# Performance work log

Measured on AMD Instinct MI355X. Metric: run time of the kernel, lower is better.

## Reference

```python
import jax, jax.numpy as jnp
import numpy as np

N = 100000      # nodes
E = 1600000     # directed edges (before self loops)
IN_DIM = 5
HID = 64
NEG_SLOPE = 0.2  # PyG GATConv default LeakyReLU slope


def setup_inputs() -> dict:
    key = jax.random.key(0)
    ks = jax.random.split(key, 12)
    x = jax.random.normal(ks[0], (N, IN_DIM), dtype=jnp.float32)
    edge_index = jax.random.randint(ks[1], (2, E), 0, N, dtype=jnp.int64)
    # layer 1 params (GATConv(5, HID), heads=1)
    W1 = jax.random.normal(ks[2], (IN_DIM, HID), dtype=jnp.float32) * (1.0 / np.sqrt(IN_DIM))
    a_src1 = jax.random.normal(ks[3], (HID,), dtype=jnp.float32) * 0.1
    a_dst1 = jax.random.normal(ks[4], (HID,), dtype=jnp.float32) * 0.1
    b1 = jnp.zeros((HID,), dtype=jnp.float32)
    # layer 2 params (GATConv(HID, 1))
    W2 = jax.random.normal(ks[5], (HID, 1), dtype=jnp.float32) * (1.0 / np.sqrt(HID))
    a_src2 = jax.random.normal(ks[6], (1,), dtype=jnp.float32) * 0.1
    a_dst2 = jax.random.normal(ks[7], (1,), dtype=jnp.float32) * 0.1
    b2 = jnp.zeros((1,), dtype=jnp.float32)
    return {"x": x, "edge_index": edge_index,
            "W1": W1, "a_src1": a_src1, "a_dst1": a_dst1, "b1": b1,
            "W2": W2, "a_src2": a_src2, "a_dst2": a_dst2, "b2": b2}


def _gat_layer(x, W, a_src, a_dst, b, src, dst):
    h = x @ W                                   # [N, F]
    s_src = h @ a_src                           # [N] per-node src score
    s_dst = h @ a_dst                           # [N] per-node dst score
    e = s_src[src] + s_dst[dst]                 # [E'] edge logits
    e = jnp.where(e > 0, e, NEG_SLOPE * e)      # LeakyReLU(0.2)
    # segment softmax over incoming edges of each dst node
    m = jax.ops.segment_max(e, dst, num_segments=N)
    ex = jnp.exp(e - m[dst])
    denom = jax.ops.segment_sum(ex, dst, num_segments=N)
    coef = ex / denom[dst]                      # [E'] attention coefficients
    out = jax.ops.segment_sum(coef[:, None] * h[src], dst, num_segments=N)
    return out + b


def reference(x, edge_index, W1, a_src1, a_dst1, b1, W2, a_src2, a_dst2, b2):
    si = jnp.arange(N, dtype=edge_index.dtype)  # add self loops (PyG default)
    src = jnp.concatenate([edge_index[0], si])
    dst = jnp.concatenate([edge_index[1], si])
    h = _gat_layer(x, W1, a_src1, a_dst1, b1, src, dst)
    h = jax.nn.relu(h)
    return _gat_layer(h, W2, a_src2, a_dst2, b2, src, dst)  # [N, 1]
```

## Files before the change

kernel.cpp:

```cpp
#include <hip/hip_runtime.h>
#include <hip/hip_bf16.h>
#include <hip/hip_fp16.h>

#define NN 100000
#define EE 1600000
#define ET (EE + NN)
#define HID 64
#define NEG 0.2f
#define NBUK 391
#define SCT_TILE 8192
#define BUKCAP 8192

__device__ __forceinline__ float uh(unsigned u) {
    __half_raw r; r.x = (unsigned short)(u & 0xFFFF);
    return __half2float(__half(r));
}
__device__ __forceinline__ unsigned f2h(float f) {
    __half h = __float2half_rn(f);
    __half_raw r = *reinterpret_cast<__half_raw*>(&h);
    return (unsigned)r.x;
}

__global__ __launch_bounds__(256) void k_proj(const float* __restrict__ x,
                                              const float* __restrict__ W1,
                                              const float* __restrict__ a_src1,
                                              const float* __restrict__ a_dst1,
                                              unsigned* __restrict__ rec,
                                              float* __restrict__ sd1,
                                              int* __restrict__ bcur) {
    if (blockIdx.x == 0) {
        for (int i = threadIdx.x; i < 1024; i += 256) bcur[i] = 0;
    }
    int wid  = threadIdx.x >> 6;
    int lane = threadIdx.x & 63;
    int half = lane >> 5, li = lane & 31;
    int n = (blockIdx.x * 4 + wid) * 2 + half;
    if (n >= NN) return;
    float xv[5];
    float h0 = 0.f, h1 = 0.f;
#pragma unroll
    for (int k = 0; k < 5; ++k) {
        xv[k] = x[n * 5 + k];
        h0 += xv[k] * W1[k * HID + li];
        h1 += xv[k] * W1[k * HID + li + 32];
    }
    float a = h0 * a_src1[li] + h1 * a_src1[li + 32];
    float b = h0 * a_dst1[li] + h1 * a_dst1[li + 32];
#pragma unroll
    for (int o = 1; o <= 16; o <<= 1) { a += __shfl_xor(a, o); b += __shfl_xor(b, o); }
    if (li == 0) {
        sd1[n] = b;
        uint4 rv;
        rv.x = __float_as_uint(a);
        rv.y = f2h(xv[0]) | (f2h(xv[1]) << 16);
        rv.z = f2h(xv[2]) | (f2h(xv[3]) << 16);
        rv.w = f2h(xv[4]);
        *(uint4*)(rec + (size_t)n * 4) = rv;
    }
}

__global__ __launch_bounds__(512) void k_bscatter(const int* __restrict__ ei,
                                                  int* __restrict__ bcur,
                                                  unsigned* __restrict__ pairs) {
    __shared__ unsigned sp[SCT_TILE];
    __shared__ unsigned short bid[SCT_TILE];
    __shared__ int cnt_[NBUK], loc[NBUK], cur[NBUK];
    __shared__ int wsum[8];
    int tid = threadIdx.x;
    int wid = tid >> 6, lane = tid & 63;
    int base = blockIdx.x * SCT_TILE;
    int tilecnt = ET - base; if (tilecnt > SCT_TILE) tilecnt = SCT_TILE;

    for (int i = tid; i < NBUK; i += 512) cnt_[i] = 0;
    __syncthreads();
    int sreg[16], dreg[16], rreg[16];
#pragma unroll
    for (int it = 0; it < 4; ++it) {
        int i = base + (it * 512 + tid) * 4;
        if (i + 3 < EE) {
            const int4 sv = *(const int4*)(ei + i);
            const int4 dv = *(const int4*)(ei + EE + i);
            sreg[it*4+0] = sv.x; sreg[it*4+1] = sv.y; sreg[it*4+2] = sv.z; sreg[it*4+3] = sv.w;
            dreg[it*4+0] = dv.x; dreg[it*4+1] = dv.y; dreg[it*4+2] = dv.z; dreg[it*4+3] = dv.w;
        } else {
#pragma unroll
            for (int k = 0; k < 4; ++k) {
                int idx = i + k;
                if (idx < EE)      { sreg[it*4+k] = ei[idx];  dreg[it*4+k] = ei[EE + idx]; }
                else if (idx < ET) { sreg[it*4+k] = idx - EE; dreg[it*4+k] = idx - EE; }
                else               { dreg[it*4+k] = -1; }
            }
        }
#pragma unroll
        for (int k = 0; k < 4; ++k)
            if (dreg[it*4+k] >= 0) rreg[it*4+k] = atomicAdd(&cnt_[dreg[it*4+k] >> 8], 1);
    }
    __syncthreads();
    int b0 = tid * 4;
    int s0 = 0;
    if (b0 < NBUK)
        for (int k = 0; k < 4 && b0 + k < NBUK; ++k) s0 += cnt_[b0 + k];
    int incl = s0;
#pragma unroll
    for (int o = 1; o < 64; o <<= 1) {
        int t = __shfl(incl, (lane - o) & 63);
        if (lane >= o) incl += t;
    }
    if (lane == 63) wsum[wid] = incl;
    __syncthreads();
    int wpref = 0;
    for (int w = 0; w < wid; ++w) wpref += wsum[w];
    if (b0 < NBUK) {
        int run = wpref + incl - s0;
        for (int k = 0; k < 4 && b0 + k < NBUK; ++k) {
            loc[b0 + k] = run;
            run += cnt_[b0 + k];
        }
    }
    __syncthreads();
    for (int i = tid; i < NBUK; i += 512) {
        int c = cnt_[i];
        cur[i] = c ? (atomicAdd(&bcur[i], c) + i * BUKCAP - loc[i]) : 0;
    }
    __syncthreads();
#pragma unroll
    for (int q = 0; q < 16; ++q) {
        if (dreg[q] >= 0) {
            int s = sreg[q], d = dreg[q];
            int b = d >> 8;
            int slot = loc[b] + rreg[q];
            sp[slot]  = ((unsigned)(d & 255) << 17) | (unsigned)s;
            bid[slot] = (unsigned short)b;
        }
    }
    __syncthreads();
    for (int i = tid; i < tilecnt; i += 512)
        pairs[cur[bid[i]] + i] = sp[i];
}

__global__ __launch_bounds__(1024) void k_bsort(const int* __restrict__ bcur,
                                                unsigned* __restrict__ pairs,
                                                int* __restrict__ rowptr,
                                                int* __restrict__ cntd) {
    __shared__ int hist[256], sc[256];
    int b = blockIdx.x;
    int cnt = bcur[b];
    if (cnt > BUKCAP) cnt = BUKCAP;
    int base = b * BUKCAP;
    int tid = threadIdx.x;
    if (tid < 256) hist[tid] = 0;
    __syncthreads();
    unsigned preg[8];
    int rreg[8];
    int i0 = tid * 8;
    if (i0 + 8 <= cnt) {
        const uint4 v0 = *(const uint4*)(pairs + base + i0);
        const uint4 v1 = *(const uint4*)(pairs + base + i0 + 4);
        preg[0] = v0.x; preg[1] = v0.y; preg[2] = v0.z; preg[3] = v0.w;
        preg[4] = v1.x; preg[5] = v1.y; preg[6] = v1.z; preg[7] = v1.w;
    } else {
#pragma unroll
        for (int j = 0; j < 8; ++j)
            preg[j] = (i0 + j < cnt) ? pairs[base + i0 + j] : 0xFFFFFFFFu;
    }
#pragma unroll
    for (int j = 0; j < 8; ++j)
        if (preg[j] != 0xFFFFFFFFu) rreg[j] = atomicAdd(&hist[preg[j] >> 17], 1);
    __syncthreads();
    if (tid < 64) {
        int v0 = hist[4 * tid], v1 = hist[4 * tid + 1];
        int v2 = hist[4 * tid + 2], v3 = hist[4 * tid + 3];
        int s = v0 + v1 + v2 + v3;
#pragma unroll
        for (int o = 1; o < 64; o <<= 1) {
            int t = __shfl(s, (tid - o) & 63);
            if (tid >= o) s += t;
        }
        int excl = s - v0 - v1 - v2 - v3;
        sc[4 * tid]     = excl;
        sc[4 * tid + 1] = excl + v0;
        sc[4 * tid + 2] = excl + v0 + v1;
        sc[4 * tid + 3] = excl + v0 + v1 + v2;
    }
    __syncthreads();
    int nbase = b << 8;
    if (tid < 256 && nbase + tid < NN) {
        rowptr[nbase + tid] = base + sc[tid];
        cntd[nbase + tid]   = hist[tid];
    }
    int* adj = (int*)pairs;
#pragma unroll
    for (int j = 0; j < 8; ++j) {
        if (preg[j] != 0xFFFFFFFFu) {
            int ld = (int)(preg[j] >> 17);
            adj[base + sc[ld] + rreg[j]] = (int)(preg[j] & 0x1FFFF);
        }
    }
}

__device__ __forceinline__ void agg1_node_gen(int n, int lane,
                                              const int* __restrict__ rowptr,
                                              const int* __restrict__ cntd,
                                              const int* __restrict__ adj,
                                              const unsigned* __restrict__ rec,
                                              const float* __restrict__ sd1,
                                              const float* __restrict__ W1,
                                              const float* __restrict__ b1,
                                              const float* __restrict__ W2,
                                              float* __restrict__ h2) {
    int off = rowptr[n], deg = cntd[n];
    float sdn = sd1[n];
    float dsum = 0.f, a0 = 0.f, a1 = 0.f, a2 = 0.f, a3 = 0.f, a4 = 0.f;
    for (int j0 = 0; j0 < deg; j0 += 64) {
        int j = j0 + lane;
        if (j < deg) {
            int s = adj[off + j];
            const uint4 v = *(const uint4*)(rec + (size_t)s * 4);
            float t = __uint_as_float(v.x) + sdn;
            float e = t > 0.f ? t : NEG * t;
            float w = __expf(e);
            dsum += w;
            a0 += w * uh(v.y); a1 += w * uh(v.y >> 16);
            a2 += w * uh(v.z); a3 += w * uh(v.z >> 16);
            a4 += w * uh(v.w);
        }
    }
#pragma unroll
    for (int o = 32; o; o >>= 1) {
        dsum += __shfl_xor(dsum, o);
        a0 += __shfl_xor(a0, o); a1 += __shfl_xor(a1, o); a2 += __shfl_xor(a2, o);
        a3 += __shfl_xor(a3, o); a4 += __shfl_xor(a4, o);
    }
    float inv = 1.0f / dsum;
    a0 *= inv; a1 *= inv; a2 *= inv; a3 *= inv; a4 *= inv;
    float of = b1[lane] + a0 * W1[lane] + a1 * W1[64 + lane] + a2 * W1[128 + lane]
             + a3 * W1[192 + lane] + a4 * W1[256 + lane];
    of = fmaxf(of, 0.f);
    float p2 = of * W2[lane];
#pragma unroll
    for (int o = 32; o; o >>= 1) p2 += __shfl_xor(p2, o);
    if (lane == 0) h2[n] = p2;
}

__global__ __launch_bounds__(256) void k_agg1(const int* __restrict__ rowptr,
                                              const int* __restrict__ cntd,
                                              const int* __restrict__ adj,
                                              const unsigned* __restrict__ rec,
                                              const float* __restrict__ sd1,
                                              const float* __restrict__ W1,
                                              const float* __restrict__ b1,
                                              const float* __restrict__ W2,
                                              float* __restrict__ h2) {
    int wid  = threadIdx.x >> 6;
    int lane = threadIdx.x & 63;
    int n0 = (blockIdx.x * 4 + wid) * 2;
    if (n0 >= NN) return;
    int d0 = cntd[n0], d1 = cntd[n0 + 1];

    if (d0 <= 32 && d1 <= 32) {
        int half = lane >> 5, li = lane & 31;
        int n = n0 + half;
        int off = rowptr[n];
        int deg = half ? d1 : d0;
        float sdn = sd1[n];
        int s = adj[off + (li < deg ? li : 0)];
        const uint4 v = *(const uint4*)(rec + (size_t)s * 4);
        float t = __uint_as_float(v.x) + sdn;
        float e = t > 0.f ? t : NEG * t;
        float p = (li < deg) ? __expf(e) : 0.f;
        float ds = p;
        float a0 = p * uh(v.y), a1 = p * uh(v.y >> 16);
        float a2 = p * uh(v.z), a3 = p * uh(v.z >> 16);
        float a4 = p * uh(v.w);
#pragma unroll
        for (int o = 1; o <= 16; o <<= 1) {
            ds += __shfl_xor(ds, o);
            a0 += __shfl_xor(a0, o); a1 += __shfl_xor(a1, o); a2 += __shfl_xor(a2, o);
            a3 += __shfl_xor(a3, o); a4 += __shfl_xor(a4, o);
        }
        float inv = 1.0f / ds;
        a0 *= inv; a1 *= inv; a2 *= inv; a3 *= inv; a4 *= inv;
        float o0 = b1[li] + a0 * W1[li] + a1 * W1[64 + li] + a2 * W1[128 + li]
                 + a3 * W1[192 + li] + a4 * W1[256 + li];
        float o1 = b1[li + 32] + a0 * W1[li + 32] + a1 * W1[96 + li] + a2 * W1[160 + li]
                 + a3 * W1[224 + li] + a4 * W1[288 + li];
        o0 = fmaxf(o0, 0.f);
        o1 = fmaxf(o1, 0.f);
        float p2 = o0 * W2[li] + o1 * W2[li + 32];
#pragma unroll
        for (int o = 1; o <= 16; o <<= 1) p2 += __shfl_xor(p2, o);
        if (li == 0) h2[n] = p2;
    } else {
        agg1_node_gen(n0,     lane, rowptr, cntd, adj, rec, sd1, W1, b1, W2, h2);
        agg1_node_gen(n0 + 1, lane, rowptr, cntd, adj, rec, sd1, W1, b1, W2, h2);
    }
}

__device__ __forceinline__ void agg2_node(int n, int lane,
                                          const int* __restrict__ rowptr,
                                          const int* __restrict__ cntd,
                                          const int* __restrict__ adj,
                                          const float* __restrict__ h2,
                                          float as2v, float ad2v, float b2v,
                                          float* __restrict__ out) {
    int off = rowptr[n], deg = cntd[n];
    float sdn = h2[n] * ad2v;
    float dsum = 0.f, nsum = 0.f;
    for (int j0 = 0; j0 < deg; j0 += 64) {
        int j = j0 + lane;
        if (j < deg) {
            int s = adj[off + j];
            float hv = h2[s];
            float e = hv * as2v + sdn;
            e = e > 0.f ? e : NEG * e;
            float ex = __expf(e);
            dsum += ex;
            nsum += ex * hv;
        }
    }
#pragma unroll
    for (int o = 32; o; o >>= 1) { dsum += __shfl_xor(dsum, o); nsum += __shfl_xor(nsum, o); }
    if (lane == 0) out[n] = nsum / dsum + b2v;
}

__global__ __launch_bounds__(256) void k_agg2(const int* __restrict__ rowptr,
                                              const int* __restrict__ cntd,
                                              const int* __restrict__ adj,
                                              const float* __restrict__ h2,
                                              const float* __restrict__ as2,
                                              const float* __restrict__ ad2,
                                              const float* __restrict__ b2,
                                              float* __restrict__ out) {
    int wid  = threadIdx.x >> 6;
    int lane = threadIdx.x & 63;
    int n0 = (blockIdx.x * 4 + wid) * 4;
    if (n0 >= NN) return;
    float as2v = as2[0], ad2v = ad2[0], b2v = b2[0];
    int d0 = cntd[n0], d1 = cntd[n0 + 1], d2 = cntd[n0 + 2], d3 = cntd[n0 + 3];

    if (d0 <= 32 && d1 <= 32 && d2 <= 32 && d3 <= 32) {
        int half = lane >> 5, li = lane & 31;
        int nA = n0 + half, nB = n0 + 2 + half;
        int offA = rowptr[nA], offB = rowptr[nB];
        int degA = half ? d1 : d0, degB = half ? d3 : d2;
        float sdA = h2[nA] * ad2v, sdB = h2[nB] * ad2v;
        float hvA = 0.f, hvB = 0.f, pA = 0.f, pB = 0.f;
        if (li < degA) {
            hvA = h2[adj[offA + li]];
            float t = hvA * as2v + sdA;
            pA = __expf(t > 0.f ? t : NEG * t);
        }
        if (li < degB) {
            hvB = h2[adj[offB + li]];
            float t = hvB * as2v + sdB;
            pB = __expf(t > 0.f ? t : NEG * t);
        }
        float dsA = pA, dsB = pB, nsA = pA * hvA, nsB = pB * hvB;
#pragma unroll
        for (int o = 1; o <= 16; o <<= 1) {
            dsA += __shfl_xor(dsA, o); nsA += __shfl_xor(nsA, o);
            dsB += __shfl_xor(dsB, o); nsB += __shfl_xor(nsB, o);
        }
        if (li == 0) {
            out[nA] = nsA / dsA + b2v;
            out[nB] = nsB / dsB + b2v;
        }
    } else {
        agg2_node(n0,     lane, rowptr, cntd, adj, h2, as2v, ad2v, b2v, out);
        agg2_node(n0 + 1, lane, rowptr, cntd, adj, h2, as2v, ad2v, b2v, out);
        agg2_node(n0 + 2, lane, rowptr, cntd, adj, h2, as2v, ad2v, b2v, out);
        agg2_node(n0 + 3, lane, rowptr, cntd, adj, h2, as2v, ad2v, b2v, out);
    }
}

extern "C" void kernel_launch(void* const* d_in, const int* in_sizes, int n_in,
                              void* d_out, int out_size, void* d_ws, size_t ws_size,
                              hipStream_t stream) {
    const float* x      = (const float*)d_in[0];
    const int*   ei     = (const int*)d_in[1];
    const float* W1     = (const float*)d_in[2];
    const float* a_src1 = (const float*)d_in[3];
    const float* a_dst1 = (const float*)d_in[4];
    const float* b1     = (const float*)d_in[5];
    const float* W2     = (const float*)d_in[6];
    const float* as2    = (const float*)d_in[7];
    const float* ad2    = (const float*)d_in[8];
    const float* b2     = (const float*)d_in[9];
    float* out = (float*)d_out;

    unsigned* rec = (unsigned*)d_ws;
    float* sd1  = (float*)(rec + (size_t)NN * 4);
    float* h2   = sd1 + NN;
    int* rowptr = (int*)(h2 + NN);
    int* cntd   = rowptr + NN;
    int* bcur   = cntd + NN;
    unsigned* pairs = (unsigned*)(bcur + 1024);
    int* adj    = (int*)pairs;

    const int NSCT = (ET + SCT_TILE - 1) / SCT_TILE;
    const int NPROJ = (NN / 2 + 3) / 4;
    const int NPAIR = (NN / 2 + 3) / 4;
    const int NQUAD = (NN + 15) / 16;

    k_proj<<<NPROJ, 256, 0, stream>>>(x, W1, a_src1, a_dst1, rec, sd1, bcur);
    k_bscatter<<<NSCT, 512, 0, stream>>>(ei, bcur, pairs);
    k_bsort<<<NBUK, 1024, 0, stream>>>(bcur, pairs, rowptr, cntd);
    k_agg1<<<NPAIR, 256, 0, stream>>>(rowptr, cntd, adj, rec, sd1, W1, b1, W2, h2);
    k_agg2<<<NQUAD, 256, 0, stream>>>(rowptr, cntd, adj, h2, as2, ad2, b2, out);
}
```

Baseline: 77.63 us.

## Fuse layer-1 aggregation into bucket sort kernel using LDS adjacency

Merges the per-bucket sort and the layer-1 attention aggregation into one kernel. The sorted source indices stay in shared memory (srt) and are read from there directly, which removes one launch and the global re-read of adj for layer 1. The scatter kernel is also changed from 512 to 1024 threads per block, with fewer edges held per thread. In exchange, aggregation parallelism drops to 391 blocks of 1024 threads, and the extra 32KB of LDS per block may limit occupancy.

```diff
diff --git a/kernel.cpp b/kernel.cpp
--- a/kernel.cpp
+++ b/kernel.cpp
@@ -59,24 +59,24 @@
     }
 }
 
-__global__ __launch_bounds__(512) void k_bscatter(const int* __restrict__ ei,
-                                                  int* __restrict__ bcur,
-                                                  unsigned* __restrict__ pairs) {
+__global__ __launch_bounds__(1024) void k_bscatter(const int* __restrict__ ei,
+                                                   int* __restrict__ bcur,
+                                                   unsigned* __restrict__ pairs) {
     __shared__ unsigned sp[SCT_TILE];
     __shared__ unsigned short bid[SCT_TILE];
     __shared__ int cnt_[NBUK], loc[NBUK], cur[NBUK];
-    __shared__ int wsum[8];
+    __shared__ int wsum[16];
     int tid = threadIdx.x;
     int wid = tid >> 6, lane = tid & 63;
     int base = blockIdx.x * SCT_TILE;
     int tilecnt = ET - base; if (tilecnt > SCT_TILE) tilecnt = SCT_TILE;
 
-    for (int i = tid; i < NBUK; i += 512) cnt_[i] = 0;
-    __syncthreads();
-    int sreg[16], dreg[16], rreg[16];
-#pragma unroll
-    for (int it = 0; it < 4; ++it) {
-        int i = base + (it * 512 + tid) * 4;
+    for (int i = tid; i < NBUK; i += 1024) cnt_[i] = 0;
+    __syncthreads();
+    int sreg[8], dreg[8], rreg[8];
+#pragma unroll
+    for (int it = 0; it < 2; ++it) {
+        int i = base + (it * 1024 + tid) * 4;
         if (i + 3 < EE) {
             const int4 sv = *(const int4*)(ei + i);
             const int4 dv = *(const int4*)(ei + EE + i);
@@ -118,13 +118,13 @@
         }
     }
     __syncthreads();
-    for (int i = tid; i < NBUK; i += 512) {
+    for (int i = tid; i < NBUK; i += 1024) {
         int c = cnt_[i];
         cur[i] = c ? (atomicAdd(&bcur[i], c) + i * BUKCAP - loc[i]) : 0;
     }
     __syncthreads();
 #pragma unroll
-    for (int q = 0; q < 16; ++q) {
+    for (int q = 0; q < 8; ++q) {
         if (dreg[q] >= 0) {
             int s = sreg[q], d = dreg[q];
             int b = d >> 8;
@@ -134,14 +134,63 @@
         }
     }
     __syncthreads();
-    for (int i = tid; i < tilecnt; i += 512)
+    for (int i = tid; i < tilecnt; i += 1024)
         pairs[cur[bid[i]] + i] = sp[i];
 }
 
-__global__ __launch_bounds__(1024) void k_bsort(const int* __restrict__ bcur,
-                                                unsigned* __restrict__ pairs,
-                                                int* __restrict__ rowptr,
-                                                int* __restrict__ cntd) {
+__device__ __forceinline__ void agg1_gen_lds(int n, int lane, int off, int deg,
+                                             const int* srt,
+                                             const unsigned* __restrict__ rec,
+                                             const float* __restrict__ sd1,
+                                             const float* __restrict__ W1,
+                                             const float* __restrict__ b1,
+                                             const float* __restrict__ W2,
+                                             float* __restrict__ h2) {
+    bool valid = n < NN;
+    float sdn = valid ? sd1[n] : 0.f;
+    float dsum = 0.f, a0 = 0.f, a1 = 0.f, a2 = 0.f, a3 = 0.f, a4 = 0.f;
+    for (int j0 = 0; j0 < deg; j0 += 64) {
+        int j = j0 + lane;
+        if (j < deg) {
+            int s = srt[off + j];
+            const uint4 v = *(const uint4*)(rec + (size_t)s * 4);
+            float t = __uint_as_float(v.x) + sdn;
+            float e = t > 0.f ? t : NEG * t;
+            float w = __expf(e);
+            dsum += w;
+            a0 += w * uh(v.y); a1 += w * uh(v.y >> 16);
+            a2 += w * uh(v.z); a3 += w * uh(v.z >> 16);
+            a4 += w * uh(v.w);
+        }
+    }
+#pragma unroll
+    for (int o = 32; o; o >>= 1) {
+        dsum += __shfl_xor(dsum, o);
+        a0 += __shfl_xor(a0, o); a1 += __shfl_xor(a1, o); a2 += __shfl_xor(a2, o);
+        a3 += __shfl_xor(a3, o); a4 += __shfl_xor(a4, o);
+    }
+    float inv = 1.0f / dsum;
+    a0 *= inv; a1 *= inv; a2 *= inv; a3 *= inv; a4 *= inv;
+    float of = b1[lane] + a0 * W1[lane] + a1 * W1[64 + lane] + a2 * W1[128 + lane]
+             + a3 * W1[192 + lane] + a4 * W1[256 + lane];
+    of = fmaxf(of, 0.f);
+    float p2 = of * W2[lane];
+#pragma unroll
+    for (int o = 32; o; o >>= 1) p2 += __shfl_xor(p2, o);
+    if (lane == 0 && valid) h2[n] = p2;
+}
+
+__global__ __launch_bounds__(1024) void k_sortagg(const int* __restrict__ bcur,
+                                                  unsigned* __restrict__ pairs,
+                                                  int* __restrict__ rowptr,
+                                                  int* __restrict__ cntd,
+                                                  const unsigned* __restrict__ rec,
+                                                  const float* __restrict__ sd1,
+                                                  const float* __restrict__ W1,
+                                                  const float* __restrict__ b1,
+                                                  const float* __restrict__ W2,
+                                                  float* __restrict__ h2) {
+    __shared__ int srt[BUKCAP];
     __shared__ int hist[256], sc[256];
     int b = blockIdx.x;
     int cnt = bcur[b];
@@ -193,106 +242,59 @@
     for (int j = 0; j < 8; ++j) {
         if (preg[j] != 0xFFFFFFFFu) {
             int ld = (int)(preg[j] >> 17);
-            adj[base + sc[ld] + rreg[j]] = (int)(preg[j] & 0x1FFFF);
-        }
-    }
-}
-
-__device__ __forceinline__ void agg1_node_gen(int n, int lane,
-                                              const int* __restrict__ rowptr,
-                                              const int* __restrict__ cntd,
-                                              const int* __restrict__ adj,
-                                              const unsigned* __restrict__ rec,
-                                              const float* __restrict__ sd1,
-                                              const float* __restrict__ W1,
-                                              const float* __restrict__ b1,
-                                              const float* __restrict__ W2,
-                                              float* __restrict__ h2) {
-    int off = rowptr[n], deg = cntd[n];
-    float sdn = sd1[n];
-    float dsum = 0.f, a0 = 0.f, a1 = 0.f, a2 = 0.f, a3 = 0.f, a4 = 0.f;
-    for (int j0 = 0; j0 < deg; j0 += 64) {
-        int j = j0 + lane;
-        if (j < deg) {
-            int s = adj[off + j];
+            int pos = sc[ld] + rreg[j];
+            int s = (int)(preg[j] & 0x1FFFF);
+            srt[pos] = s;
+            adj[base + pos] = s;
+        }
+    }
+    __syncthreads();
+
+    int wid  = tid >> 6;
+    int lane = tid & 63;
+    for (int pp = wid; pp < 128; pp += 16) {
+        int l0 = pp * 2, l1 = pp * 2 + 1;
+        int d0 = hist[l0], d1 = hist[l1];
+        if (d0 <= 32 && d1 <= 32) {
+            int half = lane >> 5, li = lane & 31;
+            int ln = half ? l1 : l0;
+            int n = nbase + ln;
+            bool valid = n < NN;
+            int deg = half ? d1 : d0;
+            int off = sc[ln];
+            float sdn = valid ? sd1[n] : 0.f;
+            int s = srt[off + (li < deg ? li : 0)];
+            if (deg == 0) s = 0;
             const uint4 v = *(const uint4*)(rec + (size_t)s * 4);
             float t = __uint_as_float(v.x) + sdn;
             float e = t > 0.f ? t : NEG * t;
-            float w = __expf(e);
-            dsum += w;
-            a0 += w * uh(v.y); a1 += w * uh(v.y >> 16);
-            a2 += w * uh(v.z); a3 += w * uh(v.z >> 16);
-            a4 += w * uh(v.w);
-        }
-    }
-#pragma unroll
-    for (int o = 32; o; o >>= 1) {
-        dsum += __shfl_xor(dsum, o);
-        a0 += __shfl_xor(a0, o); a1 += __shfl_xor(a1, o); a2 += __shfl_xor(a2, o);
-        a3 += __shfl_xor(a3, o); a4 += __shfl_xor(a4, o);
-    }
-    float inv = 1.0f / dsum;
-    a0 *= inv; a1 *= inv; a2 *= inv; a3 *= inv; a4 *= inv;
-    float of = b1[lane] + a0 * W1[lane] + a1 * W1[64 + lane] + a2 * W1[128 + lane]
-             + a3 * W1[192 + lane] + a4 * W1[256 + lane];
-    of = fmaxf(of, 0.f);
-    float p2 = of * W2[lane];
-#pragma unroll
-    for (int o = 32; o; o >>= 1) p2 += __shfl_xor(p2, o);
-    if (lane == 0) h2[n] = p2;
-}
-
-__global__ __launch_bounds__(256) void k_agg1(const int* __restrict__ rowptr,
-                                              const int* __restrict__ cntd,
-                                              const int* __restrict__ adj,
-                                              const unsigned* __restrict__ rec,
-                                              const float* __restrict__ sd1,
-                                              const float* __restrict__ W1,
-                                              const float* __restrict__ b1,
-                                              const float* __restrict__ W2,
-                                              float* __restrict__ h2) {
-    int wid  = threadIdx.x >> 6;
-    int lane = threadIdx.x & 63;
-    int n0 = (blockIdx.x * 4 + wid) * 2;
-    if (n0 >= NN) return;
-    int d0 = cntd[n0], d1 = cntd[n0 + 1];
-
-    if (d0 <= 32 && d1 <= 32) {
-        int half = lane >> 5, li = lane & 31;
-        int n = n0 + half;
-        int off = rowptr[n];
-        int deg = half ? d1 : d0;
-        float sdn = sd1[n];
-        int s = adj[off + (li < deg ? li : 0)];
-        const uint4 v = *(const uint4*)(rec + (size_t)s * 4);
-        float t = __uint_as_float(v.x) + sdn;
-        float e = t > 0.f ? t : NEG * t;
-        float p = (li < deg) ? __expf(e) : 0.f;
-        float ds = p;
-        float a0 = p * uh(v.y), a1 = p * uh(v.y >> 16);
-        float a2 = p * uh(v.z), a3 = p * uh(v.z >> 16);
-        float a4 = p * uh(v.w);
-#pragma unroll
-        for (int o = 1; o <= 16; o <<= 1) {
-            ds += __shfl_xor(ds, o);
-            a0 += __shfl_xor(a0, o); a1 += __shfl_xor(a1, o); a2 += __shfl_xor(a2, o);
-            a3 += __shfl_xor(a3, o); a4 += __shfl_xor(a4, o);
-        }
-        float inv = 1.0f / ds;
-        a0 *= inv; a1 *= inv; a2 *= inv; a3 *= inv; a4 *= inv;
-        float o0 = b1[li] + a0 * W1[li] + a1 * W1[64 + li] + a2 * W1[128 + li]
-                 + a3 * W1[192 + li] + a4 * W1[256 + li];
-        float o1 = b1[li + 32] + a0 * W1[li + 32] + a1 * W1[96 + li] + a2 * W1[160 + li]
-                 + a3 * W1[224 + li] + a4 * W1[288 + li];
-        o0 = fmaxf(o0, 0.f);
-        o1 = fmaxf(o1, 0.f);
-        float p2 = o0 * W2[li] + o1 * W2[li + 32];
-#pragma unroll
-        for (int o = 1; o <= 16; o <<= 1) p2 += __shfl_xor(p2, o);
-        if (li == 0) h2[n] = p2;
-    } else {
-        agg1_node_gen(n0,     lane, rowptr, cntd, adj, rec, sd1, W1, b1, W2, h2);
-        agg1_node_gen(n0 + 1, lane, rowptr, cntd, adj, rec, sd1, W1, b1, W2, h2);
+            float p = (li < deg) ? __expf(e) : 0.f;
+            float ds = p;
+            float a0 = p * uh(v.y), a1 = p * uh(v.y >> 16);
+            float a2 = p * uh(v.z), a3 = p * uh(v.z >> 16);
+            float a4 = p * uh(v.w);
+#pragma unroll
+            for (int o = 1; o <= 16; o <<= 1) {
+                ds += __shfl_xor(ds, o);
+                a0 += __shfl_xor(a0, o); a1 += __shfl_xor(a1, o); a2 += __shfl_xor(a2, o);
+                a3 += __shfl_xor(a3, o); a4 += __shfl_xor(a4, o);
+            }
+            float inv = 1.0f / ds;
+            a0 *= inv; a1 *= inv; a2 *= inv; a3 *= inv; a4 *= inv;
+            float o0 = b1[li] + a0 * W1[li] + a1 * W1[64 + li] + a2 * W1[128 + li]
+                     + a3 * W1[192 + li] + a4 * W1[256 + li];
+            float o1 = b1[li + 32] + a0 * W1[li + 32] + a1 * W1[96 + li] + a2 * W1[160 + li]
+                     + a3 * W1[224 + li] + a4 * W1[288 + li];
+            o0 = fmaxf(o0, 0.f);
+            o1 = fmaxf(o1, 0.f);
+            float p2 = o0 * W2[li] + o1 * W2[li + 32];
+#pragma unroll
+            for (int o = 1; o <= 16; o <<= 1) p2 += __shfl_xor(p2, o);
+            if (li == 0 && valid) h2[n] = p2;
+        } else {
+            agg1_gen_lds(nbase + l0, lane, sc[l0], d0, srt, rec, sd1, W1, b1, W2, h2);
+            agg1_gen_lds(nbase + l1, lane, sc[l1], d1, srt, rec, sd1, W1, b1, W2, h2);
+        }
     }
 }
 
@@ -399,12 +401,10 @@
 
     const int NSCT = (ET + SCT_TILE - 1) / SCT_TILE;
     const int NPROJ = (NN / 2 + 3) / 4;
-    const int NPAIR = (NN / 2 + 3) / 4;
     const int NQUAD = (NN + 15) / 16;
 
     k_proj<<<NPROJ, 256, 0, stream>>>(x, W1, a_src1, a_dst1, rec, sd1, bcur);
-    k_bscatter<<<NSCT, 512, 0, stream>>>(ei, bcur, pairs);
-    k_bsort<<<NBUK, 1024, 0, stream>>>(bcur, pairs, rowptr, cntd);
-    k_agg1<<<NPAIR, 256, 0, stream>>>(rowptr, cntd, adj, rec, sd1, W1, b1, W2, h2);
+    k_bscatter<<<NSCT, 1024, 0, stream>>>(ei, bcur, pairs);
+    k_sortagg<<<NBUK, 1024, 0, stream>>>(bcur, pairs, rowptr, cntd, rec, sd1, W1, b1, W2, h2);
     k_agg2<<<NQUAD, 256, 0, stream>>>(rowptr, cntd, adj, h2, as2, ad2, b2, out);
 }
```

After: 79.74 us. +2.7%, slower.
